# Optimization experiments

Hardware: AMD Instinct MI355X
Metric: run time of the kernel (lower is better)

Reference implementation:

```python
import jax, jax.numpy as jnp
import numpy as np

N_NODES = 100000
N_EDGES = 1600000
EMB = 128


def setup_inputs() -> dict:
    key = jax.random.key(0)
    k1, k2, k3, k4, k5, k6 = jax.random.split(key, 6)
    embeddings = jax.random.normal(k1, (N_NODES, EMB), dtype=jnp.float32)
    edge_row = jax.random.randint(k2, (N_EDGES,), 0, N_NODES, dtype=jnp.int32)
    edge_col = jax.random.randint(k3, (N_EDGES,), 0, N_NODES, dtype=jnp.int32)
    edge_val = jax.random.uniform(k4, (N_EDGES,), dtype=jnp.float32)
    W1 = jax.random.normal(k5, (EMB, EMB), dtype=jnp.float32) * (1.0 / np.sqrt(EMB))
    W2 = jax.random.normal(k6, (EMB, EMB), dtype=jnp.float32) * (1.0 / np.sqrt(EMB))
    return {"embeddings": embeddings, "edge_row": edge_row, "edge_col": edge_col,
            "edge_val": edge_val, "W1": W1, "W2": W2}


def reference(embeddings, edge_row, edge_col, edge_val, W1, W2):
    # SpMM: relevant = A @ embeddings, A in COO form (row, col, val), shape [N, N]
    gathered = embeddings[edge_col] * edge_val[:, None]          # [E, D]
    relevant = jax.ops.segment_sum(gathered, edge_row, num_segments=N_NODES)  # [N, D]
    # non-interactive + interactive messages
    non_interactive = relevant @ W1                               # [N, D]
    interactive = (relevant * embeddings) @ W2                    # [N, D]
    return non_interactive + interactive
```

## Files before the change

### kernel.cpp

```cpp
#include <hip/hip_runtime.h>
#include <hip/hip_bf16.h>
#include <stdint.h>

#define NN 100000
#define NE 1600000
#define DD 128
#define NBLK 98
#define NBKT 16
#define RPB 6250
#define NCHK 16
#define PBLK 512
#define PTHR 256
#define PCHUNK 3125
#define SEGCAP 288
#define PREPBLK 6266

typedef __attribute__((ext_vector_type(8))) short short8;
typedef __attribute__((ext_vector_type(4))) float f32x4;

__device__ inline unsigned bf16bits(float x) {
  __hip_bfloat16 h = __float2bfloat16(x);
  return (unsigned)*reinterpret_cast<unsigned short*>(&h);
}

__device__ inline float bfhi(unsigned u) { return __uint_as_float(u & 0xffff0000u); }
__device__ inline float bflo(unsigned u) { return __uint_as_float(u << 16); }

__global__ __launch_bounds__(256) void k_front(
    const int* __restrict__ row, const int* __restrict__ col,
    const float* __restrict__ val, uint2* __restrict__ ebuf,
    int* __restrict__ bcnt, const float* __restrict__ emb,
    uint4* __restrict__ tbl, const float* __restrict__ W1,
    const float* __restrict__ W2, uint4* __restrict__ wpack) {
  const int t = threadIdx.x;
  if (blockIdx.x < PBLK) {
    __shared__ int lcnt[NBKT];
    if (t < NBKT) lcnt[t] = 0;
    __syncthreads();
    const int e0 = blockIdx.x * PCHUNK;
    const size_t segbase = (size_t)blockIdx.x * NBKT * SEGCAP;
#pragma unroll 2
    for (int base = 0; base < PCHUNK; base += PTHR) {
      int off = base + t;
      if (off < PCHUNK) {
        int i = e0 + off;
        int r = row[i];
        int m = r / RPB;
        uint2 e;
        e.x = ((unsigned)col[i] << 15) | (bf16bits(val[i]) & 0x7fffu);
        e.y = (unsigned)r;
        int idx = atomicAdd(&lcnt[m], 1);
        if (idx < SEGCAP) ebuf[segbase + (size_t)m * SEGCAP + idx] = e;
      }
    }
    __syncthreads();
    if (t < NBKT) bcnt[blockIdx.x * NBKT + t] = min(lcnt[t], SEGCAP);
  } else if (blockIdx.x < PBLK + 6250) {
    int gid = (blockIdx.x - PBLK) * 256 + t;
    const float4 a = ((const float4*)emb)[2 * gid];
    const float4 b = ((const float4*)emb)[2 * gid + 1];
    uint4 u;
    u.x = bf16bits(a.x) | (bf16bits(a.y) << 16);
    u.y = bf16bits(a.z) | (bf16bits(a.w) << 16);
    u.z = bf16bits(b.x) | (bf16bits(b.y) << 16);
    u.w = bf16bits(b.z) | (bf16bits(b.w) << 16);
    tbl[gid] = u;
  } else {
    int cid = (blockIdx.x - PBLK - 6250) * 256 + t;
    int lane = cid & 63, ct = (cid >> 6) & 7, ks = cid >> 9;
    int colc = ct * 16 + (lane & 15);
    int k0 = ks * 32 + (lane >> 4) * 8;
    unsigned h[8];
#pragma unroll
    for (int j = 0; j < 8; ++j) {
      int kk = k0 + j;
      float w = (kk < DD) ? W1[kk * DD + colc] : W2[(kk - DD) * DD + colc];
      h[j] = bf16bits(w);
    }
    uint4 u;
    u.x = h[0] | (h[1] << 16);
    u.y = h[2] | (h[3] << 16);
    u.z = h[4] | (h[5] << 16);
    u.w = h[6] | (h[7] << 16);
    wpack[cid] = u;
  }
}

__global__ __launch_bounds__(1024) void k_hist(const uint2* __restrict__ ebuf,
                                               const int* __restrict__ bcnt,
                                               int* __restrict__ partial) {
  __shared__ int h[RPB];
  const int m = blockIdx.x & 15, c = blockIdx.x >> 4;
  for (int i = threadIdx.x; i < RPB; i += 1024) h[i] = 0;
  __syncthreads();
  const int base = m * RPB;
  for (int b = c * 32; b < c * 32 + 32; ++b) {
    int scnt = bcnt[b * NBKT + m];
    const uint2* src = ebuf + ((size_t)b * NBKT + m) * SEGCAP;
    for (int i = threadIdx.x; i < scnt; i += 1024)
      atomicAdd(&h[(int)src[i].y - base], 1);
  }
  __syncthreads();
  int* dst = partial + (m * NCHK + c) * RPB;
  for (int i = threadIdx.x; i < RPB; i += 1024) dst[i] = h[i];
}

__global__ __launch_bounds__(1024) void k_scan1(int* __restrict__ partial,
                                                int* __restrict__ offsets,
                                                int* __restrict__ bsum) {
  __shared__ int wsum[16];
  const int t = threadIdx.x, lane = t & 63, wid = t >> 6;
  int i = blockIdx.x * 1024 + t;
  int v = 0;
  if (i < NN) {
    int m = i / RPB, rl = i - m * RPB;
    int* p = partial + (m * NCHK) * RPB + rl;
    int s = 0;
#pragma unroll
    for (int cc = 0; cc < NCHK; ++cc) {
      int x = p[cc * RPB];
      p[cc * RPB] = s;
      s += x;
    }
    v = s;
  }
  int incl = v;
#pragma unroll
  for (int d = 1; d < 64; d <<= 1) {
    int u = __shfl_up(incl, d, 64);
    if (lane >= d) incl += u;
  }
  if (lane == 63) wsum[wid] = incl;
  __syncthreads();
  if (wid == 0) {
    int w = (lane < 16) ? wsum[lane] : 0;
#pragma unroll
    for (int d = 1; d < 16; d <<= 1) {
      int u = __shfl_up(w, d, 64);
      if (lane >= d) w += u;
    }
    if (lane < 16) wsum[lane] = w;
  }
  __syncthreads();
  int wbase = wid ? wsum[wid - 1] : 0;
  if (i < NN) offsets[i] = wbase + incl - v;
  if (t == 0) bsum[blockIdx.x] = wsum[15];
}

__global__ void k_scan2(const int* __restrict__ bsum, int* __restrict__ bpre) {
  const int lane = threadIdx.x;
  int a = bsum[lane];
  int b = (lane + 64 < NBLK) ? bsum[lane + 64] : 0;
  int sa = a, sb = b;
#pragma unroll
  for (int d = 1; d < 64; d <<= 1) {
    int u = __shfl_up(sa, d, 64);
    if (lane >= d) sa += u;
    u = __shfl_up(sb, d, 64);
    if (lane >= d) sb += u;
  }
  int totA = __shfl(sa, 63, 64);
  bpre[lane] = sa - a;
  if (lane + 64 < NBLK) bpre[lane + 64] = totA + sb - b;
}

__global__ __launch_bounds__(1024) void k_scatter3(
    const uint2* __restrict__ ebuf, const int* __restrict__ bcnt,
    const int* __restrict__ partial, const int* __restrict__ offsets,
    const int* __restrict__ bpre, unsigned* __restrict__ cpack) {
  __shared__ int cur[RPB];
  const int m = blockIdx.x & 15, c = blockIdx.x >> 4;
  const int base = m * RPB;
  const int* pre = partial + (m * NCHK + c) * RPB;
  for (int i = threadIdx.x; i < RPB; i += 1024) {
    int r = base + i;
    cur[i] = offsets[r] + bpre[r >> 10] + pre[i];
  }
  __syncthreads();
  for (int b = c * 32; b < c * 32 + 32; ++b) {
    int scnt = bcnt[b * NBKT + m];
    const uint2* src = ebuf + ((size_t)b * NBKT + m) * SEGCAP;
    for (int i = threadIdx.x; i < scnt; i += 1024) {
      uint2 e = src[i];
      int pos = atomicAdd(&cur[(int)e.y - base], 1);
      cpack[pos] = e.x;
    }
  }
}

#define CONSUME(U, W)                                          \
  {                                                            \
    float v = __uint_as_float(((U) << 16) & 0x7fff0000u);      \
    a0 = fmaf(v, bflo((W).x), a0);                             \
    a1 = fmaf(v, bfhi((W).x), a1);                             \
    a2 = fmaf(v, bflo((W).y), a2);                             \
    a3 = fmaf(v, bfhi((W).y), a3);                             \
    a4 = fmaf(v, bflo((W).z), a4);                             \
    a5 = fmaf(v, bfhi((W).z), a5);                             \
    a6 = fmaf(v, bflo((W).w), a6);                             \
    a7 = fmaf(v, bfhi((W).w), a7);                             \
  }

__global__ __launch_bounds__(512) void k_fused(
    const int* __restrict__ offsets, const int* __restrict__ bpre,
    const unsigned* __restrict__ cpack, const unsigned short* __restrict__ tbl,
    const uint4* __restrict__ wpack, float* __restrict__ out) {
  __shared__ short As[32 * 256];
  const int lane = threadIdx.x & 63;
  const int wid = threadIdx.x >> 6;
  const int q4 = lane >> 4;
  const int sub = lane & 15;
  const unsigned short* tsub = tbl + (sub << 3);

  for (int j = 0; j < 4; ++j) {
    const int r = wid * 4 + j;
    const int node = blockIdx.x * 32 + r;
    const int beg = offsets[node] + bpre[node >> 10];
    const int end = (node + 1 == NN) ? NE : offsets[node + 1] + bpre[(node + 1) >> 10];
    float a0 = 0.f, a1 = 0.f, a2 = 0.f, a3 = 0.f;
    float a4 = 0.f, a5 = 0.f, a6 = 0.f, a7 = 0.f;
    for (int j0 = beg; j0 < end; j0 += 64) {
      int idx = j0 + lane;
      unsigned pk = (idx < end) ? cpack[idx] : 0u;
      int n8 = (min(end - j0, 64) + 7) & ~7;
      unsigned uA0 = (unsigned)__shfl((int)pk, q4, 64);
      unsigned uA1 = (unsigned)__shfl((int)pk, 4 + q4, 64);
      uint4 wA0 = *(const uint4*)(tsub + ((size_t)(uA0 >> 15) << 7));
      uint4 wA1 = *(const uint4*)(tsub + ((size_t)(uA1 >> 15) << 7));
      for (int t = 8; t < n8; t += 8) {
        unsigned uB0 = (unsigned)__shfl((int)pk, t + q4, 64);
        unsigned uB1 = (unsigned)__shfl((int)pk, t + 4 + q4, 64);
        uint4 wB0 = *(const uint4*)(tsub + ((size_t)(uB0 >> 15) << 7));
        uint4 wB1 = *(const uint4*)(tsub + ((size_t)(uB1 >> 15) << 7));
        CONSUME(uA0, wA0);
        CONSUME(uA1, wA1);
        uA0 = uB0; wA0 = wB0; uA1 = uB1; wA1 = wB1;
      }
      CONSUME(uA0, wA0);
      CONSUME(uA1, wA1);
    }
    a0 += __shfl_xor(a0, 16, 64); a1 += __shfl_xor(a1, 16, 64);
    a2 += __shfl_xor(a2, 16, 64); a3 += __shfl_xor(a3, 16, 64);
    a4 += __shfl_xor(a4, 16, 64); a5 += __shfl_xor(a5, 16, 64);
    a6 += __shfl_xor(a6, 16, 64); a7 += __shfl_xor(a7, 16, 64);
    a0 += __shfl_xor(a0, 32, 64); a1 += __shfl_xor(a1, 32, 64);
    a2 += __shfl_xor(a2, 32, 64); a3 += __shfl_xor(a3, 32, 64);
    a4 += __shfl_xor(a4, 32, 64); a5 += __shfl_xor(a5, 32, 64);
    a6 += __shfl_xor(a6, 32, 64); a7 += __shfl_xor(a7, 32, 64);
    if (q4 == 0) {
      uint4 o;
      o.x = bf16bits(a0) | (bf16bits(a1) << 16);
      o.y = bf16bits(a2) | (bf16bits(a3) << 16);
      o.z = bf16bits(a4) | (bf16bits(a5) << 16);
      o.w = bf16bits(a6) | (bf16bits(a7) << 16);
      *(uint4*)(As + r * 256 + ((sub ^ (r & 7)) << 3)) = o;
    } else if (q4 == 1) {
      uint4 tw = *(const uint4*)(tbl + (size_t)node * DD + (sub << 3));
      uint4 om;
      om.x = bf16bits(a0 * bflo(tw.x)) | (bf16bits(a1 * bfhi(tw.x)) << 16);
      om.y = bf16bits(a2 * bflo(tw.y)) | (bf16bits(a3 * bfhi(tw.y)) << 16);
      om.z = bf16bits(a4 * bflo(tw.z)) | (bf16bits(a5 * bfhi(tw.z)) << 16);
      om.w = bf16bits(a6 * bflo(tw.w)) | (bf16bits(a7 * bfhi(tw.w)) << 16);
      *(uint4*)(As + r * 256 + (((16 + sub) ^ (r & 7)) << 3)) = om;
    }
  }
  __syncthreads();

  const int ct = wid;
  f32x4 acc0 = {0.f, 0.f, 0.f, 0.f};
  f32x4 acc1 = {0.f, 0.f, 0.f, 0.f};
#pragma unroll
  for (int ks = 0; ks < 8; ++ks) {
    const int slot = ks * 4 + q4;
    const int r0 = sub;
    const int r1 = sub + 16;
    short8 aT = *(const short8*)(As + r0 * 256 + ((slot ^ (r0 & 7)) << 3));
    short8 aB = *(const short8*)(As + r1 * 256 + ((slot ^ (r1 & 7)) << 3));
    short8 b = *(const short8*)(wpack + (size_t)(ks * 8 + ct) * 64 + lane);
    acc0 = __builtin_amdgcn_mfma_f32_16x16x32_bf16(aT, b, acc0, 0, 0, 0);
    acc1 = __builtin_amdgcn_mfma_f32_16x16x32_bf16(aB, b, acc1, 0, 0, 0);
  }
  const long Rb = (long)blockIdx.x * 32;
  const int ocol = ct * 16 + sub;
  const int orow = q4 * 4;
#pragma unroll
  for (int qq = 0; qq < 4; ++qq) {
    out[(Rb + orow + qq) * DD + ocol] = acc0[qq];
    out[(Rb + 16 + orow + qq) * DD + ocol] = acc1[qq];
  }
}

extern "C" void kernel_launch(void* const* d_in, const int* in_sizes, int n_in,
                              void* d_out, int out_size, void* d_ws, size_t ws_size,
                              hipStream_t stream) {
  const float* emb = (const float*)d_in[0];
  const int* erow = (const int*)d_in[1];
  const int* ecol = (const int*)d_in[2];
  const float* eva = (const float*)d_in[3];
  const float* W1 = (const float*)d_in[4];
  const float* W2 = (const float*)d_in[5];
  float* out = (float*)d_out;

  char* ws = (char*)d_ws;
  unsigned short* tbl = (unsigned short*)(ws);
  uint2* ebuf = (uint2*)(ws + 25600000);
  int* partial = (int*)(ws + 25600000 + 18874368);
  int* bcnt = (int*)(ws + 25600000 + 25274368);
  int* offsets = (int*)(ws + 51200000);
  unsigned* cpack = (unsigned*)(ws + 52000128);
  int* bsum = (int*)(ws + 58400128);
  int* bpre = (int*)(ws + 58400640);
  uint4* wpack = (uint4*)(ws + 58401152);

  k_front<<<PBLK + PREPBLK, 256, 0, stream>>>(erow, ecol, eva, ebuf, bcnt,
                                              emb, (uint4*)tbl, W1, W2, wpack);
  k_hist<<<NBKT * NCHK, 1024, 0, stream>>>(ebuf, bcnt, partial);
  k_scan1<<<NBLK, 1024, 0, stream>>>(partial, offsets, bsum);
  k_scan2<<<1, 64, 0, stream>>>(bsum, bpre);
  k_scatter3<<<NBKT * NCHK, 1024, 0, stream>>>(ebuf, bcnt, partial, offsets, bpre, cpack);
  k_fused<<<NN / 32, 512, 0, stream>>>(offsets, bpre, cpack, tbl, wpack, out);
}
```

Baseline: 131.5 us.

## Double histogram chunks, assign one wave per edge segment, store partials as u16

Splits each bucket's histogram and scatter work into twice as many blocks (NCHK 16→32), with each 64-lane wave in a block handling one edge segment instead of the whole block looping over 32 segments. Partial counts are stored as 16-bit values, so the partial array keeps the same size despite twice as many chunks. The aim is more blocks in flight for the histogram/scatter phases, plus less per-block serial looping. In exchange the scan1 kernel reads twice as many partial entries, and the 16-bit storage assumes per-chunk prefix counts fit in a ushort.

```diff
diff --git a/kernel.cpp b/kernel.cpp
--- a/kernel.cpp
+++ b/kernel.cpp
@@ -8,7 +8,7 @@
 #define NBLK 98
 #define NBKT 16
 #define RPB 6250
-#define NCHK 16
+#define NCHK 32
 #define PBLK 512
 #define PTHR 256
 #define PCHUNK 3125
@@ -88,24 +88,24 @@
 
 __global__ __launch_bounds__(1024) void k_hist(const uint2* __restrict__ ebuf,
                                                const int* __restrict__ bcnt,
-                                               int* __restrict__ partial) {
+                                               unsigned short* __restrict__ partial) {
   __shared__ int h[RPB];
   const int m = blockIdx.x & 15, c = blockIdx.x >> 4;
+  const int tb = threadIdx.x >> 6, lane = threadIdx.x & 63;
   for (int i = threadIdx.x; i < RPB; i += 1024) h[i] = 0;
   __syncthreads();
   const int base = m * RPB;
-  for (int b = c * 32; b < c * 32 + 32; ++b) {
-    int scnt = bcnt[b * NBKT + m];
-    const uint2* src = ebuf + ((size_t)b * NBKT + m) * SEGCAP;
-    for (int i = threadIdx.x; i < scnt; i += 1024)
-      atomicAdd(&h[(int)src[i].y - base], 1);
-  }
-  __syncthreads();
-  int* dst = partial + (m * NCHK + c) * RPB;
-  for (int i = threadIdx.x; i < RPB; i += 1024) dst[i] = h[i];
-}
-
-__global__ __launch_bounds__(1024) void k_scan1(int* __restrict__ partial,
+  const int b = c * 16 + tb;
+  const int scnt = bcnt[b * NBKT + m];
+  const uint2* src = ebuf + ((size_t)b * NBKT + m) * SEGCAP;
+  for (int i = lane; i < scnt; i += 64)
+    atomicAdd(&h[(int)src[i].y - base], 1);
+  __syncthreads();
+  unsigned short* dst = partial + (size_t)(m * NCHK + c) * RPB;
+  for (int i = threadIdx.x; i < RPB; i += 1024) dst[i] = (unsigned short)h[i];
+}
+
+__global__ __launch_bounds__(1024) void k_scan1(unsigned short* __restrict__ partial,
                                                 int* __restrict__ offsets,
                                                 int* __restrict__ bsum) {
   __shared__ int wsum[16];
@@ -114,12 +114,12 @@
   int v = 0;
   if (i < NN) {
     int m = i / RPB, rl = i - m * RPB;
-    int* p = partial + (m * NCHK) * RPB + rl;
+    unsigned short* p = partial + (size_t)(m * NCHK) * RPB + rl;
     int s = 0;
 #pragma unroll
     for (int cc = 0; cc < NCHK; ++cc) {
-      int x = p[cc * RPB];
-      p[cc * RPB] = s;
+      int x = p[(size_t)cc * RPB];
+      p[(size_t)cc * RPB] = (unsigned short)s;
       s += x;
     }
     v = s;
@@ -166,25 +166,25 @@
 
 __global__ __launch_bounds__(1024) void k_scatter3(
     const uint2* __restrict__ ebuf, const int* __restrict__ bcnt,
-    const int* __restrict__ partial, const int* __restrict__ offsets,
+    const unsigned short* __restrict__ partial, const int* __restrict__ offsets,
     const int* __restrict__ bpre, unsigned* __restrict__ cpack) {
   __shared__ int cur[RPB];
   const int m = blockIdx.x & 15, c = blockIdx.x >> 4;
+  const int tb = threadIdx.x >> 6, lane = threadIdx.x & 63;
   const int base = m * RPB;
-  const int* pre = partial + (m * NCHK + c) * RPB;
+  const unsigned short* pre = partial + (size_t)(m * NCHK + c) * RPB;
   for (int i = threadIdx.x; i < RPB; i += 1024) {
     int r = base + i;
     cur[i] = offsets[r] + bpre[r >> 10] + pre[i];
   }
   __syncthreads();
-  for (int b = c * 32; b < c * 32 + 32; ++b) {
-    int scnt = bcnt[b * NBKT + m];
-    const uint2* src = ebuf + ((size_t)b * NBKT + m) * SEGCAP;
-    for (int i = threadIdx.x; i < scnt; i += 1024) {
-      uint2 e = src[i];
-      int pos = atomicAdd(&cur[(int)e.y - base], 1);
-      cpack[pos] = e.x;
-    }
+  const int b = c * 16 + tb;
+  const int scnt = bcnt[b * NBKT + m];
+  const uint2* src = ebuf + ((size_t)b * NBKT + m) * SEGCAP;
+  for (int i = lane; i < scnt; i += 64) {
+    uint2 e = src[i];
+    int pos = atomicAdd(&cur[(int)e.y - base], 1);
+    cpack[pos] = e.x;
   }
 }
 
@@ -304,7 +304,7 @@
   char* ws = (char*)d_ws;
   unsigned short* tbl = (unsigned short*)(ws);
   uint2* ebuf = (uint2*)(ws + 25600000);
-  int* partial = (int*)(ws + 25600000 + 18874368);
+  unsigned short* partial = (unsigned short*)(ws + 25600000 + 18874368);
   int* bcnt = (int*)(ws + 25600000 + 25274368);
   int* offsets = (int*)(ws + 51200000);
   unsigned* cpack = (unsigned*)(ws + 52000128);
```

Measured after the change: 120.2 us. 1.09x faster.
